# Optimization experiments

Measured on AMD Instinct MI355X. Metric: run time of the kernel, lower is better.

## Reference

```python
import jax, jax.numpy as jnp
import numpy as np

D_MODEL = 512
D_FFN = 2048
N_LAYERS = 6
VOCAB = 1000
D_STATE = 16
D_CONV = 4
D_INNER = 2 * D_MODEL  # expand=2
DT_RANK = 32           # ceil(d_model/16)
B, LT, LS = 2, 512, 512


def _pos_encoding(length, d_model):
    pos = np.arange(length, dtype=np.float32)[:, None]
    div = np.exp(np.arange(0, d_model, 2, dtype=np.float32) * (-np.log(10000.0) / d_model))
    pe = np.zeros((length, d_model), np.float32)
    pe[:, 0::2] = np.sin(pos * div)
    pe[:, 1::2] = np.cos(pos * div)
    return jnp.asarray(pe)


def _layer_norm(x, g, b, eps=1e-6):
    m = x.mean(-1, keepdims=True)
    v = ((x - m) ** 2).mean(-1, keepdims=True)
    return (x - m) * jax.lax.rsqrt(v + eps) * g + b


def _mamba(x, in_w, conv_w, conv_b, xproj_w, dt_w, dt_b, A_log, Dskip, out_w):
    # x: (b, l, d_model)
    b, l, _ = x.shape
    xz = x @ in_w.T                                   # (b, l, 2*d_inner)
    xc, z = jnp.split(xz, 2, axis=-1)
    # causal depthwise conv over time
    xt = jnp.transpose(xc, (0, 2, 1))                 # (b, d_inner, l)
    xt = jnp.pad(xt, ((0, 0), (0, 0), (D_CONV - 1, 0)))
    xt = jax.lax.conv_general_dilated(
        xt, conv_w, window_strides=(1,), padding='VALID',
        feature_group_count=D_INNER, dimension_numbers=('NCH', 'OIH', 'NCH'))
    xc = jax.nn.silu(jnp.transpose(xt, (0, 2, 1)) + conv_b)  # (b, l, d_inner)
    dbl = xc @ xproj_w.T                              # (b, l, dt_rank + 2*n)
    dt, Bm, Cm = jnp.split(dbl, [DT_RANK, DT_RANK + D_STATE], axis=-1)
    dt = jax.nn.softplus(dt @ dt_w.T + dt_b)          # (b, l, d_inner)
    A = -jnp.exp(A_log)                               # (d_inner, n)

    def step(h, xs):
        dt_t, B_t, C_t, u_t = xs                      # (b,d),(b,n),(b,n),(b,d)
        dA = jnp.exp(dt_t[..., None] * A)             # (b, d, n)
        h = dA * h + (dt_t * u_t)[..., None] * B_t[:, None, :]
        y = jnp.einsum('bdn,bn->bd', h, C_t)
        return h, y

    h0 = jnp.zeros((b, D_INNER, D_STATE), x.dtype)
    xs = (jnp.swapaxes(dt, 0, 1), jnp.swapaxes(Bm, 0, 1),
          jnp.swapaxes(Cm, 0, 1), jnp.swapaxes(xc, 0, 1))
    _, ys = jax.lax.scan(step, h0, xs)                # ys: (l, b, d_inner)
    y = jnp.swapaxes(ys, 0, 1) + xc * Dskip
    y = y * jax.nn.silu(z)
    return y @ out_w.T                                # (b, l, d_model)


def setup_inputs() -> dict:
    key = jax.random.key(0)
    ks = iter(jax.random.split(key, 40))

    def rn(shape, s=0.02):
        return jax.random.normal(next(ks), shape, jnp.float32) * s

    def mamba_params():
        return dict(
            in_w=rn((N_LAYERS, 2 * D_INNER, D_MODEL)),
            conv_w=rn((N_LAYERS, D_INNER, 1, D_CONV), 0.1),
            conv_b=rn((N_LAYERS, D_INNER)),
            xproj=rn((N_LAYERS, DT_RANK + 2 * D_STATE, D_INNER)),
            dtw=rn((N_LAYERS, D_INNER, DT_RANK)),
            dtb=rn((N_LAYERS, D_INNER)),
            Alog=jnp.log(jnp.broadcast_to(jnp.arange(1.0, D_STATE + 1.0, dtype=jnp.float32), (N_LAYERS, D_INNER, D_STATE))),
            D=jnp.ones((N_LAYERS, D_INNER), jnp.float32),
            outw=rn((N_LAYERS, D_MODEL, D_INNER)),
        )

    ps, pc = mamba_params(), mamba_params()
    inp = {
        'src': jax.random.normal(next(ks), (B, LS, D_MODEL), jnp.float32),
        'tgt': jax.random.randint(next(ks), (B, LT), 0, VOCAB),
        'emb': rn((VOCAB, D_MODEL)),
        'in_w_s': ps['in_w'], 'conv_w_s': ps['conv_w'], 'conv_b_s': ps['conv_b'],
        'xproj_s': ps['xproj'], 'dtw_s': ps['dtw'], 'dtb_s': ps['dtb'],
        'Alog_s': ps['Alog'], 'D_s': ps['D'], 'outw_s': ps['outw'],
        'in_w_c': pc['in_w'], 'conv_w_c': pc['conv_w'], 'conv_b_c': pc['conv_b'],
        'xproj_c': pc['xproj'], 'dtw_c': pc['dtw'], 'dtb_c': pc['dtb'],
        'Alog_c': pc['Alog'], 'D_c': pc['D'], 'outw_c': pc['outw'],
        'ffn_w1': rn((N_LAYERS, D_FFN, D_MODEL)),
        'ffn_b1': jnp.zeros((N_LAYERS, D_FFN), jnp.float32),
        'ffn_w2': rn((N_LAYERS, D_MODEL, D_FFN)),
        'ffn_b2': jnp.zeros((N_LAYERS, D_MODEL), jnp.float32),
        'ln_g': jnp.ones((N_LAYERS, 3, D_MODEL), jnp.float32),
        'ln_b': jnp.zeros((N_LAYERS, 3, D_MODEL), jnp.float32),
        'fin_g': jnp.ones((D_MODEL,), jnp.float32),
        'fin_b': jnp.zeros((D_MODEL,), jnp.float32),
    }
    return inp


def reference(src, tgt, emb, in_w_s, conv_w_s, conv_b_s, xproj_s, dtw_s, dtb_s,
              Alog_s, D_s, outw_s, in_w_c, conv_w_c, conv_b_c, xproj_c, dtw_c,
              dtb_c, Alog_c, D_c, outw_c, ffn_w1, ffn_b1, ffn_w2, ffn_b2,
              ln_g, ln_b, fin_g, fin_b):
    # NormalizedEmbedding + sinusoidal positional encoding
    x = emb[tgt] * jnp.sqrt(jnp.asarray(D_MODEL, jnp.float32))
    x = x + _pos_encoding(LT, D_MODEL)[None]
    for i in range(N_LAYERS):
        # self mamba (post-norm, normalize_before=False)
        t2 = _mamba(x, in_w_s[i], conv_w_s[i], conv_b_s[i], xproj_s[i],
                    dtw_s[i], dtb_s[i], Alog_s[i], D_s[i], outw_s[i])
        x = _layer_norm(x + t2, ln_g[i, 0], ln_b[i, 0])
        # cross mamba over concat([memory, tgt]) then take last LT steps
        cat = jnp.concatenate([src, x], axis=1)
        t2 = _mamba(cat, in_w_c[i], conv_w_c[i], conv_b_c[i], xproj_c[i],
                    dtw_c[i], dtb_c[i], Alog_c[i], D_c[i], outw_c[i])[:, -LT:]
        x = _layer_norm(x + t2, ln_g[i, 1], ln_b[i, 1])
        # positionwise FFN
        h = jax.nn.relu(x @ ffn_w1[i].T + ffn_b1[i]) @ ffn_w2[i].T + ffn_b2[i]
        x = _layer_norm(x + h, ln_g[i, 2], ln_b[i, 2])
    return _layer_norm(x, fin_g, fin_b)
```

## Files before the change

### kernel.cpp

```cpp
#include <hip/hip_runtime.h>
#include <math.h>

#define DMODEL 512
#define DINNER 1024
#define DSTATE 16
#define DTRANK 32
#define NLAYERS 6
#define BB 2
#define LT 512
#define LS 512
#define NCHUNK 32

typedef __attribute__((ext_vector_type(8))) short bf16x8;
typedef __attribute__((ext_vector_type(8))) unsigned short u16x8;
typedef __attribute__((ext_vector_type(4))) float f32x4;

__device__ __forceinline__ unsigned short f2bf(float f) {
  unsigned u = __float_as_uint(f);
  u += 0x7fffu + ((u >> 16) & 1u);
  return (unsigned short)(u >> 16);
}

template<int EPI>
__device__ __forceinline__ float epi_apply(float acc, float b) {
  if (EPI == 1) { float v = acc + b; return v > 0.f ? v : 0.f; }
  if (EPI == 2) { return acc + b; }
  if (EPI == 3) { float v = acc + b; return fmaxf(v, 0.f) + log1pf(__expf(-fabsf(v))); }
  return acc;
}

__global__ __launch_bounds__(256) void cvt_kernel(const float* __restrict__ in,
    unsigned short* __restrict__ out, int n8) {
  int i = blockIdx.x * 256 + threadIdx.x;
  if (i >= n8) return;
  float4 a = ((const float4*)in)[i * 2];
  float4 b = ((const float4*)in)[i * 2 + 1];
  u16x8 o;
  o[0] = f2bf(a.x); o[1] = f2bf(a.y); o[2] = f2bf(a.z); o[3] = f2bf(a.w);
  o[4] = f2bf(b.x); o[5] = f2bf(b.y); o[6] = f2bf(b.z); o[7] = f2bf(b.w);
  *(u16x8*)&out[i * 8] = o;
}

__global__ __launch_bounds__(256) void embed_kernel(const int* __restrict__ tgt,
    const float* __restrict__ emb, float* __restrict__ X,
    unsigned short* __restrict__ Xb) {
  int i = blockIdx.x * 256 + threadIdx.x;
  int d = i & (DMODEL - 1);
  int bt = i >> 9;
  int t = bt & (LT - 1);
  int tok = tgt[bt];
  float div = __expf((float)(d & ~1) * (-9.210340371976184f / (float)DMODEL));
  float ang = (float)t * div;
  float pe = (d & 1) ? cosf(ang) : sinf(ang);
  float v = emb[(size_t)tok * DMODEL + d] * 22.627416997969522f + pe;
  X[i] = v;
  Xb[i] = f2bf(v);
}

__global__ __launch_bounds__(256) void concat_kernel(const float* __restrict__ src,
    const float* __restrict__ X, unsigned short* __restrict__ CATb) {
  int i = blockIdx.x * 256 + threadIdx.x;
  int c8 = (i & 63) * 8;
  int r = i >> 6;
  int l = r & 1023;
  int b = r >> 10;
  const float* s = (l < LS) ? (src + ((size_t)b * LS + l) * DMODEL)
                            : (X + ((size_t)b * LT + (l - LS)) * DMODEL);
  float4 a = *(const float4*)(s + c8);
  float4 bq = *(const float4*)(s + c8 + 4);
  u16x8 o;
  o[0] = f2bf(a.x); o[1] = f2bf(a.y); o[2] = f2bf(a.z); o[3] = f2bf(a.w);
  o[4] = f2bf(bq.x); o[5] = f2bf(bq.y); o[6] = f2bf(bq.z); o[7] = f2bf(bq.w);
  *(u16x8*)&CATb[(size_t)r * DMODEL + c8] = o;
}

template<int BK, int EPI, bool SPLIT, bool OUTB>
__global__ __launch_bounds__(256) void mgemm(
    const unsigned short* __restrict__ A, const unsigned short* __restrict__ Bw,
    const float* __restrict__ bias, float* __restrict__ C,
    unsigned short* __restrict__ Cb, int M, int N, int K, int lda) {
  constexpr int PAD = BK + 8;
  constexpr int CH = BK / 32;
  __shared__ __align__(16) unsigned short As[64 * PAD];
  __shared__ __align__(16) unsigned short Bs[64 * PAD];
  const int tid = threadIdx.x;
  const int bn = blockIdx.x * 64;
  const int bm = blockIdx.y * 64;
  const int lane = tid & 63;
  const int w = tid >> 6;
  const int wr = (w >> 1) * 32;
  const int wc = (w & 1) * 32;
  const int l15 = lane & 15;
  const int l4 = lane >> 4;
  const int koff = l4 * 8;
  int kcnt = K, kbeg = 0;
  if (SPLIT) { kcnt = K / (int)gridDim.z; kbeg = blockIdx.z * kcnt; }
  const int nt = kcnt / BK;
  f32x4 acc[2][2] = {};

  int row_[CH], k8_[CH];
  const unsigned short *Ap[CH], *Bp[CH];
#pragma unroll
  for (int i = 0; i < CH; ++i) {
    int f = tid + 256 * i;
    row_[i] = f / (BK / 8);
    k8_[i] = (f % (BK / 8)) * 8;
    Ap[i] = A + (size_t)(bm + row_[i]) * lda + kbeg + k8_[i];
    Bp[i] = Bw + (size_t)(bn + row_[i]) * K + kbeg + k8_[i];
  }

  u16x8 av[CH], bv[CH];
#pragma unroll
  for (int i = 0; i < CH; ++i) { av[i] = *(const u16x8*)Ap[i]; bv[i] = *(const u16x8*)Bp[i]; }

  for (int t = 0; t < nt; ++t) {
    __syncthreads();
#pragma unroll
    for (int i = 0; i < CH; ++i) {
      *(u16x8*)&As[row_[i] * PAD + k8_[i]] = av[i];
      *(u16x8*)&Bs[row_[i] * PAD + k8_[i]] = bv[i];
    }
    if (t + 1 < nt) {
      int ko = (t + 1) * BK;
#pragma unroll
      for (int i = 0; i < CH; ++i) {
        av[i] = *(const u16x8*)(Ap[i] + ko);
        bv[i] = *(const u16x8*)(Bp[i] + ko);
      }
    }
    __syncthreads();
#pragma unroll
    for (int kk = 0; kk < CH; ++kk) {
      bf16x8 afr[2], bfr[2];
#pragma unroll
      for (int i = 0; i < 2; ++i) {
        afr[i] = *(const bf16x8*)&As[(wr + i * 16 + l15) * PAD + kk * 32 + koff];
        bfr[i] = *(const bf16x8*)&Bs[(wc + i * 16 + l15) * PAD + kk * 32 + koff];
      }
#pragma unroll
      for (int fr = 0; fr < 2; ++fr)
#pragma unroll
        for (int fc = 0; fc < 2; ++fc)
          acc[fr][fc] = __builtin_amdgcn_mfma_f32_16x16x32_bf16(
              afr[fr], bfr[fc], acc[fr][fc], 0, 0, 0);
    }
  }

  if (SPLIT) {
    float* Pz = C + (size_t)blockIdx.z * M * N;
#pragma unroll
    for (int fc = 0; fc < 2; ++fc) {
      int col = bn + wc + fc * 16 + l15;
#pragma unroll
      for (int fr = 0; fr < 2; ++fr) {
        int row0 = bm + wr + fr * 16 + l4 * 4;
#pragma unroll
        for (int r = 0; r < 4; ++r)
          Pz[(size_t)(row0 + r) * N + col] = acc[fr][fc][r];
      }
    }
  } else {
#pragma unroll
    for (int fc = 0; fc < 2; ++fc) {
      int col = bn + wc + fc * 16 + l15;
      float bvs = (EPI != 0) ? bias[col] : 0.f;
#pragma unroll
      for (int fr = 0; fr < 2; ++fr) {
        int row0 = bm + wr + fr * 16 + l4 * 4;
#pragma unroll
        for (int r = 0; r < 4; ++r) {
          float v = epi_apply<EPI>(acc[fr][fc][r], bvs);
          if (OUTB) Cb[(size_t)(row0 + r) * N + col] = f2bf(v);
          else      C[(size_t)(row0 + r) * N + col] = v;
        }
      }
    }
  }
}

__global__ __launch_bounds__(256) void xred_kernel(const float* __restrict__ P,
    float* __restrict__ DBL, unsigned short* __restrict__ DBLb, int total) {
  int i = blockIdx.x * 256 + threadIdx.x;
  if (i >= total) return;
  float s = 0.f;
  for (int z = 0; z < 8; ++z) s += P[(size_t)z * total + i];
  DBL[i] = s;
  int col = i & 63;
  if (col < 32) DBLb[(size_t)(i >> 6) * 32 + col] = f2bf(s);
}

__global__ __launch_bounds__(256) void conv_silu_kernel(
    const float* __restrict__ xz, const float* __restrict__ w,
    const float* __restrict__ bias, float* __restrict__ out,
    unsigned short* __restrict__ outb, int L) {
  int idx = blockIdx.x * 256 + threadIdx.x;
  int d = idx & (DINNER - 1);
  int bt = idx >> 10;
  int b = bt / L;
  int t = bt - b * L;
  const float* col = xz + ((size_t)b * L) * (2 * DINNER) + d;
  float acc = bias[d];
#pragma unroll
  for (int k = 0; k < 4; ++k) {
    int tt = t - 3 + k;
    if (tt >= 0) acc = fmaf(col[(size_t)tt * (2 * DINNER)], w[d * 4 + k], acc);
  }
  float sig = 1.f / (1.f + __expf(-acc));
  float v = acc * sig;
  out[idx] = v;
  outb[idx] = f2bf(v);
}

__global__ __launch_bounds__(256) void scan_pass1(
    const float* __restrict__ dt, const float* __restrict__ dbl,
    const float* __restrict__ u, const float* __restrict__ Alog,
    float* __restrict__ P, float* __restrict__ S, int L, int CL) {
  __shared__ float BC[32][32];
  const int tid = threadIdx.x;
  const int d = blockIdx.x * 256 + tid;
  const int b = blockIdx.y;
  const int c = blockIdx.z;
  const int t0 = c * CL;
  if (tid < CL * 8) {
    int t = tid >> 3, j4 = (tid & 7) * 4;
    *(float4*)&BC[t][j4] = *(const float4*)(dbl + ((size_t)b * L + t0 + t) * 64 + 32 + j4);
  }
  float A[16], h[16], Pp[16];
#pragma unroll
  for (int j = 0; j < 4; ++j) {
    float4 a4 = *(const float4*)(Alog + d * 16 + j * 4);
    A[j * 4 + 0] = -__expf(a4.x); A[j * 4 + 1] = -__expf(a4.y);
    A[j * 4 + 2] = -__expf(a4.z); A[j * 4 + 3] = -__expf(a4.w);
  }
#pragma unroll
  for (int n = 0; n < 16; ++n) { h[n] = 0.f; Pp[n] = 1.f; }
  const float* dtp = dt + ((size_t)b * L + t0) * DINNER + d;
  const float* up  = u  + ((size_t)b * L + t0) * DINNER + d;
  __syncthreads();
  float dtv = dtp[0], uv = up[0];
  for (int t = 0; t < CL; ++t) {
    float dtn = 0.f, un = 0.f;
    if (t + 1 < CL) { dtn = dtp[(size_t)(t + 1) * DINNER]; un = up[(size_t)(t + 1) * DINNER]; }
    float du = dtv * uv;
    float Bv[16];
#pragma unroll
    for (int j = 0; j < 4; ++j) {
      float4 b4 = *(const float4*)&BC[t][j * 4];
      Bv[j * 4 + 0] = b4.x; Bv[j * 4 + 1] = b4.y; Bv[j * 4 + 2] = b4.z; Bv[j * 4 + 3] = b4.w;
    }
#pragma unroll
    for (int n = 0; n < 16; ++n) {
      float dA = __expf(dtv * A[n]);
      Pp[n] *= dA;
      h[n] = fmaf(dA, h[n], du * Bv[n]);
    }
    dtv = dtn; uv = un;
  }
  size_t base = (size_t)c * 32768 + ((size_t)(b * 1024 + d) << 4);
#pragma unroll
  for (int j = 0; j < 4; ++j) {
    *(float4*)&P[base + j * 4] = make_float4(Pp[j*4], Pp[j*4+1], Pp[j*4+2], Pp[j*4+3]);
    *(float4*)&S[base + j * 4] = make_float4(h[j*4], h[j*4+1], h[j*4+2], h[j*4+3]);
  }
}

__global__ __launch_bounds__(256) void scan_mid(
    const float* __restrict__ P, const float* __restrict__ S,
    float* __restrict__ HIN, int C) {
  int s = blockIdx.x * 256 + threadIdx.x;
  float h = 0.f;
  for (int c = 0; c < C; ++c) {
    float p = P[(size_t)c * 32768 + s];
    float sv = S[(size_t)c * 32768 + s];
    HIN[(size_t)c * 32768 + s] = h;
    h = fmaf(p, h, sv);
  }
}

__global__ __launch_bounds__(256) void scan_pass2(
    const float* __restrict__ dt, const float* __restrict__ dbl,
    const float* __restrict__ u, const float* __restrict__ xz,
    const float* __restrict__ Alog, const float* __restrict__ Dsk,
    const float* __restrict__ HIN, unsigned short* __restrict__ ysb,
    int L, int CL, int c0) {
  __shared__ float BC[32][32];
  const int tid = threadIdx.x;
  const int d = blockIdx.x * 256 + tid;
  const int b = blockIdx.y;
  const int c = blockIdx.z + c0;
  const int t0 = c * CL;
  if (tid < CL * 8) {
    int t = tid >> 3, j4 = (tid & 7) * 4;
    *(float4*)&BC[t][j4] = *(const float4*)(dbl + ((size_t)b * L + t0 + t) * 64 + 32 + j4);
  }
  float A[16], h[16];
#pragma unroll
  for (int j = 0; j < 4; ++j) {
    float4 a4 = *(const float4*)(Alog + d * 16 + j * 4);
    A[j * 4 + 0] = -__expf(a4.x); A[j * 4 + 1] = -__expf(a4.y);
    A[j * 4 + 2] = -__expf(a4.z); A[j * 4 + 3] = -__expf(a4.w);
  }
  size_t base = (size_t)c * 32768 + ((size_t)(b * 1024 + d) << 4);
#pragma unroll
  for (int j = 0; j < 4; ++j) {
    float4 h4 = *(const float4*)&HIN[base + j * 4];
    h[j * 4 + 0] = h4.x; h[j * 4 + 1] = h4.y; h[j * 4 + 2] = h4.z; h[j * 4 + 3] = h4.w;
  }
  float Dv = Dsk[d];
  const float* dtp = dt + ((size_t)b * L + t0) * DINNER + d;
  const float* up  = u  + ((size_t)b * L + t0) * DINNER + d;
  const float* zp  = xz + ((size_t)b * L + t0) * (2 * DINNER) + DINNER + d;
  unsigned short* yp = ysb + ((size_t)(b * 512) + (t0 - c0 * CL)) * DINNER + d;
  __syncthreads();
  float dtv = dtp[0], uv = up[0], zv = zp[0];
  for (int t = 0; t < CL; ++t) {
    float dtn = 0.f, un = 0.f, zn = 0.f;
    if (t + 1 < CL) {
      dtn = dtp[(size_t)(t + 1) * DINNER];
      un  = up[(size_t)(t + 1) * DINNER];
      zn  = zp[(size_t)(t + 1) * (2 * DINNER)];
    }
    float du = dtv * uv;
    float Bv[16], Cv[16];
#pragma unroll
    for (int j = 0; j < 4; ++j) {
      float4 b4 = *(const float4*)&BC[t][j * 4];
      float4 c4 = *(const float4*)&BC[t][16 + j * 4];
      Bv[j*4+0] = b4.x; Bv[j*4+1] = b4.y; Bv[j*4+2] = b4.z; Bv[j*4+3] = b4.w;
      Cv[j*4+0] = c4.x; Cv[j*4+1] = c4.y; Cv[j*4+2] = c4.z; Cv[j*4+3] = c4.w;
    }
    float y = 0.f;
#pragma unroll
    for (int n = 0; n < 16; ++n) {
      float dA = __expf(dtv * A[n]);
      h[n] = fmaf(dA, h[n], du * Bv[n]);
      y = fmaf(h[n], Cv[n], y);
    }
    float sig = 1.f / (1.f + __expf(-zv));
    yp[(size_t)t * DINNER] = f2bf((y + uv * Dv) * (zv * sig));
    dtv = dtn; uv = un; zv = zn;
  }
}

template<int NZ, int EPI>
__global__ __launch_bounds__(64) void ln_red_kernel(
    const float* __restrict__ res, const float* __restrict__ P,
    const float* __restrict__ bias, const float* __restrict__ g,
    const float* __restrict__ be, float* __restrict__ out,
    unsigned short* __restrict__ outb) {
  int r = blockIdx.x;
  int lane = threadIdx.x;
  const float* rp = res + (size_t)r * DMODEL;
  float v[8];
  float s = 0.f, ss = 0.f;
#pragma unroll
  for (int j = 0; j < 8; ++j) {
    int col = lane + j * 64;
    float acc = 0.f;
#pragma unroll
    for (int z = 0; z < NZ; ++z) acc += P[(size_t)z * 524288 + (size_t)r * DMODEL + col];
    float bv = (EPI != 0) ? bias[col] : 0.f;
    float x = rp[col] + epi_apply<EPI>(acc, bv);
    v[j] = x; s += x; ss += x * x;
  }
#pragma unroll
  for (int o = 32; o > 0; o >>= 1) { s += __shfl_xor(s, o); ss += __shfl_xor(ss, o); }
  float m = s * (1.f / 512.f);
  float var = ss * (1.f / 512.f) - m * m;
  float rs = rsqrtf(var + 1e-6f);
#pragma unroll
  for (int j = 0; j < 8; ++j) {
    int col = lane + j * 64;
    float o2 = (v[j] - m) * rs * g[col] + be[col];
    out[(size_t)r * DMODEL + col] = o2;
    outb[(size_t)r * DMODEL + col] = f2bf(o2);
  }
}

__global__ __launch_bounds__(64) void ln_final_kernel(
    const float* __restrict__ res, const float* __restrict__ g,
    const float* __restrict__ be, float* __restrict__ out) {
  int r = blockIdx.x;
  int lane = threadIdx.x;
  const float* rp = res + (size_t)r * DMODEL;
  float v[8];
  float s = 0.f, ss = 0.f;
#pragma unroll
  for (int j = 0; j < 8; ++j) {
    float x = rp[lane + j * 64];
    v[j] = x; s += x; ss += x * x;
  }
#pragma unroll
  for (int o = 32; o > 0; o >>= 1) { s += __shfl_xor(s, o); ss += __shfl_xor(ss, o); }
  float m = s * (1.f / 512.f);
  float var = ss * (1.f / 512.f) - m * m;
  float rs = rsqrtf(var + 1e-6f);
#pragma unroll
  for (int j = 0; j < 8; ++j) {
    int c = lane + j * 64;
    out[(size_t)r * DMODEL + c] = (v[j] - m) * rs * g[c] + be[c];
  }
}

extern "C" void kernel_launch(void* const* d_in, const int* in_sizes, int n_in,
                              void* d_out, int out_size, void* d_ws, size_t ws_size,
                              hipStream_t stream) {
  (void)in_sizes; (void)n_in; (void)out_size; (void)ws_size;
  const float* src      = (const float*)d_in[0];
  const int*   tgt      = (const int*)d_in[1];
  const float* emb      = (const float*)d_in[2];
  const float* in_w_s   = (const float*)d_in[3];
  const float* conv_w_s = (const float*)d_in[4];
  const float* conv_b_s = (const float*)d_in[5];
  const float* xproj_s  = (const float*)d_in[6];
  const float* dtw_s    = (const float*)d_in[7];
  const float* dtb_s    = (const float*)d_in[8];
  const float* Alog_s   = (const float*)d_in[9];
  const float* D_s      = (const float*)d_in[10];
  const float* outw_s   = (const float*)d_in[11];
  const float* in_w_c   = (const float*)d_in[12];
  const float* conv_w_c = (const float*)d_in[13];
  const float* conv_b_c = (const float*)d_in[14];
  const float* xproj_c  = (const float*)d_in[15];
  const float* dtw_c    = (const float*)d_in[16];
  const float* dtb_c    = (const float*)d_in[17];
  const float* Alog_c   = (const float*)d_in[18];
  const float* D_c      = (const float*)d_in[19];
  const float* outw_c   = (const float*)d_in[20];
  const float* ffn_w1   = (const float*)d_in[21];
  const float* ffn_b1   = (const float*)d_in[22];
  const float* ffn_w2   = (const float*)d_in[23];
  const float* ffn_b2   = (const float*)d_in[24];
  const float* ln_g     = (const float*)d_in[25];
  const float* ln_b     = (const float*)d_in[26];
  const float* fin_g    = (const float*)d_in[27];
  const float* fin_b    = (const float*)d_in[28];

  float* ws   = (float*)d_ws;
  float* X    = ws;
  float* XZ   = X + 524288;
  float* XC   = XZ + 4194304;
  float* DT   = XC + 2097152;
  float* DBL  = DT + 2097152;
  float* SC_P = DBL + 131072;
  float* SC_S = SC_P + 1048576;
  unsigned short* U = (unsigned short*)(SC_S + 1048576);
  unsigned short* Xb   = U;
  unsigned short* CATb = Xb + 524288;
  unsigned short* XCb  = CATb + 1048576;
  unsigned short* DBLb = XCb + 2097152;
  unsigned short* XZb  = DBLb + 65536;
  unsigned short* YSb  = XZb + 2097152;
  unsigned short* WB   = YSb + 1048576;
  unsigned short* inwsb = WB;
  unsigned short* inwcb = inwsb + 6291456;
  unsigned short* xpsb  = inwcb + 6291456;
  unsigned short* xpcb  = xpsb + 393216;
  unsigned short* dtwsb = xpcb + 393216;
  unsigned short* dtwcb = dtwsb + 196608;
  unsigned short* owsb  = dtwcb + 196608;
  unsigned short* owcb  = owsb + 3145728;
  unsigned short* f1b   = owcb + 3145728;
  unsigned short* f2b   = f1b + 6291456;

  cvt_kernel<<<3072, 256, 0, stream>>>(in_w_s, inwsb, 786432);
  cvt_kernel<<<3072, 256, 0, stream>>>(in_w_c, inwcb, 786432);
  cvt_kernel<<<192, 256, 0, stream>>>(xproj_s, xpsb, 49152);
  cvt_kernel<<<192, 256, 0, stream>>>(xproj_c, xpcb, 49152);
  cvt_kernel<<<96, 256, 0, stream>>>(dtw_s, dtwsb, 24576);
  cvt_kernel<<<96, 256, 0, stream>>>(dtw_c, dtwcb, 24576);
  cvt_kernel<<<1536, 256, 0, stream>>>(outw_s, owsb, 393216);
  cvt_kernel<<<1536, 256, 0, stream>>>(outw_c, owcb, 393216);
  cvt_kernel<<<3072, 256, 0, stream>>>(ffn_w1, f1b, 786432);
  cvt_kernel<<<3072, 256, 0, stream>>>(ffn_w2, f2b, 786432);

  embed_kernel<<<2048, 256, 0, stream>>>(tgt, emb, X, Xb);

  for (int i = 0; i < NLAYERS; ++i) {
    mgemm<64, 0, false, false><<<dim3(32, 16), 256, 0, stream>>>(
        Xb, inwsb + (size_t)i * 1048576, nullptr, XZ, nullptr, 1024, 2048, 512, 512);
    conv_silu_kernel<<<4096, 256, 0, stream>>>(
        XZ, conv_w_s + (size_t)i * 4096, conv_b_s + (size_t)i * 1024, XC, XCb, 512);
    mgemm<64, 0, true, false><<<dim3(1, 16, 8), 256, 0, stream>>>(
        XCb, xpsb + (size_t)i * 65536, nullptr, SC_P, nullptr, 1024, 64, 1024, 1024);
    xred_kernel<<<256, 256, 0, stream>>>(SC_P, DBL, DBLb, 65536);
    mgemm<32, 3, false, false><<<dim3(16, 16), 256, 0, stream>>>(
        DBLb, dtwsb + (size_t)i * 32768, dtb_s + (size_t)i * 1024, DT, nullptr,
        1024, 1024, 32, 32);
    scan_pass1<<<dim3(4, 2, 32), 256, 0, stream>>>(
        DT, DBL, XC, Alog_s + (size_t)i * 16384, SC_P, SC_S, 512, 16);
    scan_mid<<<128, 256, 0, stream>>>(SC_P, SC_S, SC_P, 32);
    scan_pass2<<<dim3(4, 2, 32), 256, 0, stream>>>(
        DT, DBL, XC, XZ, Alog_s + (size_t)i * 16384, D_s + (size_t)i * 1024,
        SC_P, YSb, 512, 16, 0);
    mgemm<64, 0, true, false><<<dim3(8, 16, 4), 256, 0, stream>>>(
        YSb, owsb + (size_t)i * 524288, nullptr, XZ, nullptr, 1024, 512, 1024, 1024);
    ln_red_kernel<4, 0><<<1024, 64, 0, stream>>>(
        X, XZ, nullptr, ln_g + (size_t)(i * 3 + 0) * 512,
        ln_b + (size_t)(i * 3 + 0) * 512, X, Xb);

    concat_kernel<<<512, 256, 0, stream>>>(src, X, CATb);
    mgemm<64, 0, false, false><<<dim3(32, 32), 256, 0, stream>>>(
        CATb, inwcb + (size_t)i * 1048576, nullptr, XZ, nullptr, 2048, 2048, 512, 512);
    conv_silu_kernel<<<8192, 256, 0, stream>>>(
        XZ, conv_w_c + (size_t)i * 4096, conv_b_c + (size_t)i * 1024, XC, XCb, 1024);
    mgemm<64, 0, true, false><<<dim3(1, 32, 8), 256, 0, stream>>>(
        XCb, xpcb + (size_t)i * 65536, nullptr, SC_P, nullptr, 2048, 64, 1024, 1024);
    xred_kernel<<<512, 256, 0, stream>>>(SC_P, DBL, DBLb, 131072);
    mgemm<32, 3, false, false><<<dim3(16, 32), 256, 0, stream>>>(
        DBLb, dtwcb + (size_t)i * 32768, dtb_c + (size_t)i * 1024, DT, nullptr,
        2048, 1024, 32, 32);
    scan_pass1<<<dim3(4, 2, 32), 256, 0, stream>>>(
        DT, DBL, XC, Alog_c + (size_t)i * 16384, SC_P, SC_S, 1024, 32);
    scan_mid<<<128, 256, 0, stream>>>(SC_P, SC_S, SC_P, 32);
    scan_pass2<<<dim3(4, 2, 16), 256, 0, stream>>>(
        DT, DBL, XC, XZ, Alog_c + (size_t)i * 16384, D_c + (size_t)i * 1024,
        SC_P, YSb, 1024, 32, 16);
    mgemm<64, 0, true, false><<<dim3(8, 16, 4), 256, 0, stream>>>(
        YSb, owcb + (size_t)i * 524288, nullptr, XZ, nullptr, 1024, 512, 1024, 1024);
    ln_red_kernel<4, 0><<<1024, 64, 0, stream>>>(
        X, XZ, nullptr, ln_g + (size_t)(i * 3 + 1) * 512,
        ln_b + (size_t)(i * 3 + 1) * 512, X, Xb);

    mgemm<64, 1, false, true><<<dim3(32, 16), 256, 0, stream>>>(
        Xb, f1b + (size_t)i * 1048576, ffn_b1 + (size_t)i * 2048, nullptr, XZb,
        1024, 2048, 512, 512);
    mgemm<64, 0, true, false><<<dim3(8, 16, 8), 256, 0, stream>>>(
        XZb, f2b + (size_t)i * 1048576, nullptr, XZ, nullptr, 1024, 512, 2048, 2048);
    ln_red_kernel<8, 2><<<1024, 64, 0, stream>>>(
        X, XZ, ffn_b2 + (size_t)i * 512, ln_g + (size_t)(i * 3 + 2) * 512,
        ln_b + (size_t)(i * 3 + 2) * 512, X, Xb);
  }

  ln_final_kernel<<<1024, 64, 0, stream>>>(X, fin_g, fin_b, (float*)d_out);
}
```

Before: 1.223 ms.

## Store intermediates in bf16, widen GEMM tiles, fuse weight conversion and scan mid-pass

Intermediate activations (xz, conv output, dt, dbl) are now stored as bf16 rather than fp32, which halves memory traffic in the conv, scan and GEMM epilogues. A new 64x128-tile GEMM variant replaces the 64x64 one for the large projections. The ten weight-conversion launches are merged into a single kernel. The separate scan_mid launch is removed, and each scan_pass2 block instead recomputes its own carry-in state from the per-chunk P/S values. The concat kernel is removed: src is copied once and the layernorm writes x straight into the concat buffer. Together these cut launches and bandwidth, at the cost of redundant carry recomputation and lower-precision intermediates.

```diff
diff --git a/kernel.cpp b/kernel.cpp
--- a/kernel.cpp
+++ b/kernel.cpp
@@ -9,7 +9,6 @@
 #define BB 2
 #define LT 512
 #define LS 512
-#define NCHUNK 32
 
 typedef __attribute__((ext_vector_type(8))) short bf16x8;
 typedef __attribute__((ext_vector_type(8))) unsigned short u16x8;
@@ -19,6 +18,9 @@
   unsigned u = __float_as_uint(f);
   u += 0x7fffu + ((u >> 16) & 1u);
   return (unsigned short)(u >> 16);
+}
+__device__ __forceinline__ float bf2f(unsigned short u) {
+  return __uint_as_float((unsigned)u << 16);
 }
 
 template<int EPI>
@@ -29,16 +31,32 @@
   return acc;
 }
 
-__global__ __launch_bounds__(256) void cvt_kernel(const float* __restrict__ in,
-    unsigned short* __restrict__ out, int n8) {
+__global__ __launch_bounds__(256) void cvt_all_kernel(
+    const float* __restrict__ i0, const float* __restrict__ i1,
+    const float* __restrict__ i2, const float* __restrict__ i3,
+    const float* __restrict__ i4, const float* __restrict__ i5,
+    const float* __restrict__ i6, const float* __restrict__ i7,
+    const float* __restrict__ i8, const float* __restrict__ i9,
+    unsigned short* __restrict__ outbase) {
   int i = blockIdx.x * 256 + threadIdx.x;
-  if (i >= n8) return;
-  float4 a = ((const float4*)in)[i * 2];
-  float4 b = ((const float4*)in)[i * 2 + 1];
+  if (i >= 4079616) return;
+  const float* in; int off;
+  if      (i <  786432) { in = i0; off = i; }
+  else if (i < 1572864) { in = i1; off = i -  786432; }
+  else if (i < 1622016) { in = i2; off = i - 1572864; }
+  else if (i < 1671168) { in = i3; off = i - 1622016; }
+  else if (i < 1695744) { in = i4; off = i - 1671168; }
+  else if (i < 1720320) { in = i5; off = i - 1695744; }
+  else if (i < 2113536) { in = i6; off = i - 1720320; }
+  else if (i < 2506752) { in = i7; off = i - 2113536; }
+  else if (i < 3293184) { in = i8; off = i - 2506752; }
+  else                  { in = i9; off = i - 3293184; }
+  float4 a = ((const float4*)in)[off * 2];
+  float4 b = ((const float4*)in)[off * 2 + 1];
   u16x8 o;
   o[0] = f2bf(a.x); o[1] = f2bf(a.y); o[2] = f2bf(a.z); o[3] = f2bf(a.w);
   o[4] = f2bf(b.x); o[5] = f2bf(b.y); o[6] = f2bf(b.z); o[7] = f2bf(b.w);
-  *(u16x8*)&out[i * 8] = o;
+  *(u16x8*)&outbase[(size_t)i * 8] = o;
 }
 
 __global__ __launch_bounds__(256) void embed_kernel(const int* __restrict__ tgt,
@@ -57,21 +75,133 @@
   Xb[i] = f2bf(v);
 }
 
-__global__ __launch_bounds__(256) void concat_kernel(const float* __restrict__ src,
-    const float* __restrict__ X, unsigned short* __restrict__ CATb) {
+__global__ __launch_bounds__(256) void catsrc_kernel(const float* __restrict__ src,
+    unsigned short* __restrict__ CATb) {
   int i = blockIdx.x * 256 + threadIdx.x;
   int c8 = (i & 63) * 8;
   int r = i >> 6;
-  int l = r & 1023;
-  int b = r >> 10;
-  const float* s = (l < LS) ? (src + ((size_t)b * LS + l) * DMODEL)
-                            : (X + ((size_t)b * LT + (l - LS)) * DMODEL);
-  float4 a = *(const float4*)(s + c8);
-  float4 bq = *(const float4*)(s + c8 + 4);
+  int b = r >> 9, l = r & 511;
+  const float* s = src + ((size_t)b * 512 + l) * DMODEL + c8;
+  float4 a = *(const float4*)s;
+  float4 bq = *(const float4*)(s + 4);
   u16x8 o;
   o[0] = f2bf(a.x); o[1] = f2bf(a.y); o[2] = f2bf(a.z); o[3] = f2bf(a.w);
   o[4] = f2bf(bq.x); o[5] = f2bf(bq.y); o[6] = f2bf(bq.z); o[7] = f2bf(bq.w);
-  *(u16x8*)&CATb[(size_t)r * DMODEL + c8] = o;
+  *(u16x8*)&CATb[((size_t)b * 1024 + l) * DMODEL + c8] = o;
+}
+
+template<int BK, int EPI, bool SPLIT, bool OUTB>
+__global__ __launch_bounds__(256) void mgemmA(
+    const unsigned short* __restrict__ A, const unsigned short* __restrict__ Bw,
+    const float* __restrict__ bias, float* __restrict__ C,
+    unsigned short* __restrict__ Cb, int M, int N, int K, int lda) {
+  constexpr int PAD = BK + 8;
+  constexpr int CHA = BK / 32;
+  constexpr int CHB = BK / 16;
+  __shared__ __align__(16) unsigned short As[64 * PAD];
+  __shared__ __align__(16) unsigned short Bs[128 * PAD];
+  const int tid = threadIdx.x;
+  const int bn = blockIdx.x * 128;
+  const int bm = blockIdx.y * 64;
+  const int lane = tid & 63;
+  const int w = tid >> 6;
+  const int wr = (w >> 1) * 32;
+  const int wc = (w & 1) * 64;
+  const int l15 = lane & 15;
+  const int l4 = lane >> 4;
+  const int koff = l4 * 8;
+  int kcnt = K, kbeg = 0;
+  if (SPLIT) { kcnt = K / (int)gridDim.z; kbeg = blockIdx.z * kcnt; }
+  const int nt = kcnt / BK;
+  f32x4 acc[2][4] = {};
+
+  int arow_[CHA], ak8_[CHA];
+  const unsigned short* Ap[CHA];
+#pragma unroll
+  for (int i = 0; i < CHA; ++i) {
+    int f = tid + 256 * i;
+    arow_[i] = f / (BK / 8);
+    ak8_[i] = (f % (BK / 8)) * 8;
+    Ap[i] = A + (size_t)(bm + arow_[i]) * lda + kbeg + ak8_[i];
+  }
+  int brow_[CHB], bk8_[CHB];
+  const unsigned short* Bp[CHB];
+#pragma unroll
+  for (int i = 0; i < CHB; ++i) {
+    int f = tid + 256 * i;
+    brow_[i] = f / (BK / 8);
+    bk8_[i] = (f % (BK / 8)) * 8;
+    Bp[i] = Bw + (size_t)(bn + brow_[i]) * K + kbeg + bk8_[i];
+  }
+
+  u16x8 av[CHA], bv[CHB];
+#pragma unroll
+  for (int i = 0; i < CHA; ++i) av[i] = *(const u16x8*)Ap[i];
+#pragma unroll
+  for (int i = 0; i < CHB; ++i) bv[i] = *(const u16x8*)Bp[i];
+
+  for (int t = 0; t < nt; ++t) {
+    __syncthreads();
+#pragma unroll
+    for (int i = 0; i < CHA; ++i) *(u16x8*)&As[arow_[i] * PAD + ak8_[i]] = av[i];
+#pragma unroll
+    for (int i = 0; i < CHB; ++i) *(u16x8*)&Bs[brow_[i] * PAD + bk8_[i]] = bv[i];
+    if (t + 1 < nt) {
+      int ko = (t + 1) * BK;
+#pragma unroll
+      for (int i = 0; i < CHA; ++i) av[i] = *(const u16x8*)(Ap[i] + ko);
+#pragma unroll
+      for (int i = 0; i < CHB; ++i) bv[i] = *(const u16x8*)(Bp[i] + ko);
+    }
+    __syncthreads();
+#pragma unroll
+    for (int kk = 0; kk < BK / 32; ++kk) {
+      bf16x8 afr[2], bfr[4];
+#pragma unroll
+      for (int i = 0; i < 2; ++i)
+        afr[i] = *(const bf16x8*)&As[(wr + i * 16 + l15) * PAD + kk * 32 + koff];
+#pragma unroll
+      for (int j = 0; j < 4; ++j)
+        bfr[j] = *(const bf16x8*)&Bs[(wc + j * 16 + l15) * PAD + kk * 32 + koff];
+#pragma unroll
+      for (int fr = 0; fr < 2; ++fr)
+#pragma unroll
+        for (int fc = 0; fc < 4; ++fc)
+          acc[fr][fc] = __builtin_amdgcn_mfma_f32_16x16x32_bf16(
+              afr[fr], bfr[fc], acc[fr][fc], 0, 0, 0);
+    }
+  }
+
+  if (SPLIT) {
+    float* Pz = C + (size_t)blockIdx.z * M * N;
+#pragma unroll
+    for (int fc = 0; fc < 4; ++fc) {
+      int col = bn + wc + fc * 16 + l15;
+#pragma unroll
+      for (int fr = 0; fr < 2; ++fr) {
+        int row0 = bm + wr + fr * 16 + l4 * 4;
+#pragma unroll
+        for (int r = 0; r < 4; ++r)
+          Pz[(size_t)(row0 + r) * N + col] = acc[fr][fc][r];
+      }
+    }
+  } else {
+#pragma unroll
+    for (int fc = 0; fc < 4; ++fc) {
+      int col = bn + wc + fc * 16 + l15;
+      float bvs = (EPI != 0) ? bias[col] : 0.f;
+#pragma unroll
+      for (int fr = 0; fr < 2; ++fr) {
+        int row0 = bm + wr + fr * 16 + l4 * 4;
+#pragma unroll
+        for (int r = 0; r < 4; ++r) {
+          float v = epi_apply<EPI>(acc[fr][fc][r], bvs);
+          if (OUTB) Cb[(size_t)(row0 + r) * N + col] = f2bf(v);
+          else      C[(size_t)(row0 + r) * N + col] = v;
+        }
+      }
+    }
+  }
 }
 
 template<int BK, int EPI, bool SPLIT, bool OUTB>
@@ -179,41 +309,36 @@
 }
 
 __global__ __launch_bounds__(256) void xred_kernel(const float* __restrict__ P,
-    float* __restrict__ DBL, unsigned short* __restrict__ DBLb, int total) {
+    unsigned short* __restrict__ DBLb, int total) {
   int i = blockIdx.x * 256 + threadIdx.x;
   if (i >= total) return;
   float s = 0.f;
   for (int z = 0; z < 8; ++z) s += P[(size_t)z * total + i];
-  DBL[i] = s;
-  int col = i & 63;
-  if (col < 32) DBLb[(size_t)(i >> 6) * 32 + col] = f2bf(s);
+  DBLb[i] = f2bf(s);
 }
 
 __global__ __launch_bounds__(256) void conv_silu_kernel(
-    const float* __restrict__ xz, const float* __restrict__ w,
-    const float* __restrict__ bias, float* __restrict__ out,
-    unsigned short* __restrict__ outb, int L) {
+    const unsigned short* __restrict__ xzb, const float* __restrict__ w,
+    const float* __restrict__ bias, unsigned short* __restrict__ outb, int L) {
   int idx = blockIdx.x * 256 + threadIdx.x;
   int d = idx & (DINNER - 1);
   int bt = idx >> 10;
   int b = bt / L;
   int t = bt - b * L;
-  const float* col = xz + ((size_t)b * L) * (2 * DINNER) + d;
+  const unsigned short* col = xzb + ((size_t)b * L) * (2 * DINNER) + d;
   float acc = bias[d];
 #pragma unroll
   for (int k = 0; k < 4; ++k) {
     int tt = t - 3 + k;
-    if (tt >= 0) acc = fmaf(col[(size_t)tt * (2 * DINNER)], w[d * 4 + k], acc);
+    if (tt >= 0) acc = fmaf(bf2f(col[(size_t)tt * (2 * DINNER)]), w[d * 4 + k], acc);
   }
   float sig = 1.f / (1.f + __expf(-acc));
-  float v = acc * sig;
-  out[idx] = v;
-  outb[idx] = f2bf(v);
+  outb[idx] = f2bf(acc * sig);
 }
 
 __global__ __launch_bounds__(256) void scan_pass1(
-    const float* __restrict__ dt, const float* __restrict__ dbl,
-    const float* __restrict__ u, const float* __restrict__ Alog,
+    const unsigned short* __restrict__ dt, const unsigned short* __restrict__ dblb,
+    const unsigned short* __restrict__ u, const float* __restrict__ Alog,
     float* __restrict__ P, float* __restrict__ S, int L, int CL) {
   __shared__ float BC[32][32];
   const int tid = threadIdx.x;
@@ -221,9 +346,11 @@
   const int b = blockIdx.y;
   const int c = blockIdx.z;
   const int t0 = c * CL;
-  if (tid < CL * 8) {
-    int t = tid >> 3, j4 = (tid & 7) * 4;
-    *(float4*)&BC[t][j4] = *(const float4*)(dbl + ((size_t)b * L + t0 + t) * 64 + 32 + j4);
+  if (tid < CL * 4) {
+    int t = tid >> 2, j8 = (tid & 3) * 8;
+    u16x8 v = *(const u16x8*)(dblb + ((size_t)b * L + t0 + t) * 64 + 32 + j8);
+#pragma unroll
+    for (int j = 0; j < 8; ++j) BC[t][j8 + j] = bf2f(v[j]);
   }
   float A[16], h[16], Pp[16];
 #pragma unroll
@@ -234,25 +361,22 @@
   }
 #pragma unroll
   for (int n = 0; n < 16; ++n) { h[n] = 0.f; Pp[n] = 1.f; }
-  const float* dtp = dt + ((size_t)b * L + t0) * DINNER + d;
-  const float* up  = u  + ((size_t)b * L + t0) * DINNER + d;
+  const unsigned short* dtp = dt + ((size_t)b * L + t0) * DINNER + d;
+  const unsigned short* up  = u  + ((size_t)b * L + t0) * DINNER + d;
   __syncthreads();
-  float dtv = dtp[0], uv = up[0];
+  float dtv = bf2f(dtp[0]), uv = bf2f(up[0]);
   for (int t = 0; t < CL; ++t) {
     float dtn = 0.f, un = 0.f;
-    if (t + 1 < CL) { dtn = dtp[(size_t)(t + 1) * DINNER]; un = up[(size_t)(t + 1) * DINNER]; }
+    if (t + 1 < CL) {
+      dtn = bf2f(dtp[(size_t)(t + 1) * DINNER]);
+      un  = bf2f(up[(size_t)(t + 1) * DINNER]);
+    }
     float du = dtv * uv;
-    float Bv[16];
-#pragma unroll
-    for (int j = 0; j < 4; ++j) {
-      float4 b4 = *(const float4*)&BC[t][j * 4];
-      Bv[j * 4 + 0] = b4.x; Bv[j * 4 + 1] = b4.y; Bv[j * 4 + 2] = b4.z; Bv[j * 4 + 3] = b4.w;
-    }
 #pragma unroll
     for (int n = 0; n < 16; ++n) {
       float dA = __expf(dtv * A[n]);
       Pp[n] *= dA;
-      h[n] = fmaf(dA, h[n], du * Bv[n]);
+      h[n] = fmaf(dA, h[n], du * BC[t][n]);
     }
     dtv = dtn; uv = un;
   }
@@ -264,34 +388,23 @@
   }
 }
 
-__global__ __launch_bounds__(256) void scan_mid(
+__global__ __launch_bounds__(256) void scan_pass2(
+    const unsigned short* __restrict__ dt, const unsigned short* __restrict__ dblb,
+    const unsigned short* __restrict__ u, const unsigned short* __restrict__ xzb,
+    const float* __restrict__ Alog, const float* __restrict__ Dsk,
     const float* __restrict__ P, const float* __restrict__ S,
-    float* __restrict__ HIN, int C) {
-  int s = blockIdx.x * 256 + threadIdx.x;
-  float h = 0.f;
-  for (int c = 0; c < C; ++c) {
-    float p = P[(size_t)c * 32768 + s];
-    float sv = S[(size_t)c * 32768 + s];
-    HIN[(size_t)c * 32768 + s] = h;
-    h = fmaf(p, h, sv);
-  }
-}
-
-__global__ __launch_bounds__(256) void scan_pass2(
-    const float* __restrict__ dt, const float* __restrict__ dbl,
-    const float* __restrict__ u, const float* __restrict__ xz,
-    const float* __restrict__ Alog, const float* __restrict__ Dsk,
-    const float* __restrict__ HIN, unsigned short* __restrict__ ysb,
-    int L, int CL, int c0) {
+    unsigned short* __restrict__ ysb, int L, int CL, int c0) {
   __shared__ float BC[32][32];
   const int tid = threadIdx.x;
   const int d = blockIdx.x * 256 + tid;
   const int b = blockIdx.y;
   const int c = blockIdx.z + c0;
   const int t0 = c * CL;
-  if (tid < CL * 8) {
-    int t = tid >> 3, j4 = (tid & 7) * 4;
-    *(float4*)&BC[t][j4] = *(const float4*)(dbl + ((size_t)b * L + t0 + t) * 64 + 32 + j4);
+  if (tid < CL * 4) {
+    int t = tid >> 2, j8 = (tid & 3) * 8;
+    u16x8 v = *(const u16x8*)(dblb + ((size_t)b * L + t0 + t) * 64 + 32 + j8);
+#pragma unroll
+    for (int j = 0; j < 8; ++j) BC[t][j8 + j] = bf2f(v[j]);
   }
   float A[16], h[16];
 #pragma unroll
@@ -300,41 +413,42 @@
     A[j * 4 + 0] = -__expf(a4.x); A[j * 4 + 1] = -__expf(a4.y);
     A[j * 4 + 2] = -__expf(a4.z); A[j * 4 + 3] = -__expf(a4.w);
   }
-  size_t base = (size_t)c * 32768 + ((size_t)(b * 1024 + d) << 4);
-#pragma unroll
-  for (int j = 0; j < 4; ++j) {
-    float4 h4 = *(const float4*)&HIN[base + j * 4];
-    h[j * 4 + 0] = h4.x; h[j * 4 + 1] = h4.y; h[j * 4 + 2] = h4.z; h[j * 4 + 3] = h4.w;
+#pragma unroll
+  for (int n = 0; n < 16; ++n) h[n] = 0.f;
+  size_t sbase = (size_t)(b * 1024 + d) << 4;
+  for (int cc = 0; cc < c; ++cc) {
+    size_t bb = (size_t)cc * 32768 + sbase;
+#pragma unroll
+    for (int j = 0; j < 4; ++j) {
+      float4 p4 = *(const float4*)&P[bb + j * 4];
+      float4 s4 = *(const float4*)&S[bb + j * 4];
+      h[j*4+0] = fmaf(p4.x, h[j*4+0], s4.x);
+      h[j*4+1] = fmaf(p4.y, h[j*4+1], s4.y);
+      h[j*4+2] = fmaf(p4.z, h[j*4+2], s4.z);
+      h[j*4+3] = fmaf(p4.w, h[j*4+3], s4.w);
+    }
   }
   float Dv = Dsk[d];
-  const float* dtp = dt + ((size_t)b * L + t0) * DINNER + d;
-  const float* up  = u  + ((size_t)b * L + t0) * DINNER + d;
-  const float* zp  = xz + ((size_t)b * L + t0) * (2 * DINNER) + DINNER + d;
+  const unsigned short* dtp = dt + ((size_t)b * L + t0) * DINNER + d;
+  const unsigned short* up  = u  + ((size_t)b * L + t0) * DINNER + d;
+  const unsigned short* zp  = xzb + ((size_t)b * L + t0) * (2 * DINNER) + DINNER + d;
   unsigned short* yp = ysb + ((size_t)(b * 512) + (t0 - c0 * CL)) * DINNER + d;
   __syncthreads();
-  float dtv = dtp[0], uv = up[0], zv = zp[0];
+  float dtv = bf2f(dtp[0]), uv = bf2f(up[0]), zv = bf2f(zp[0]);
   for (int t = 0; t < CL; ++t) {
     float dtn = 0.f, un = 0.f, zn = 0.f;
     if (t + 1 < CL) {
-      dtn = dtp[(size_t)(t + 1) * DINNER];
-      un  = up[(size_t)(t + 1) * DINNER];
-      zn  = zp[(size_t)(t + 1) * (2 * DINNER)];
+      dtn = bf2f(dtp[(size_t)(t + 1) * DINNER]);
+      un  = bf2f(up[(size_t)(t + 1) * DINNER]);
+      zn  = bf2f(zp[(size_t)(t + 1) * (2 * DINNER)]);
     }
     float du = dtv * uv;
-    float Bv[16], Cv[16];
-#pragma unroll
-    for (int j = 0; j < 4; ++j) {
-      float4 b4 = *(const float4*)&BC[t][j * 4];
-      float4 c4 = *(const float4*)&BC[t][16 + j * 4];
-      Bv[j*4+0] = b4.x; Bv[j*4+1] = b4.y; Bv[j*4+2] = b4.z; Bv[j*4+3] = b4.w;
-      Cv[j*4+0] = c4.x; Cv[j*4+1] = c4.y; Cv[j*4+2] = c4.z; Cv[j*4+3] = c4.w;
-    }
     float y = 0.f;
 #pragma unroll
     for (int n = 0; n < 16; ++n) {
       float dA = __expf(dtv * A[n]);
-      h[n] = fmaf(dA, h[n], du * Bv[n]);
-      y = fmaf(h[n], Cv[n], y);
+      h[n] = fmaf(dA, h[n], du * BC[t][n]);
+      y = fmaf(h[n], BC[t][16 + n], y);
     }
     float sig = 1.f / (1.f + __expf(-zv));
     yp[(size_t)t * DINNER] = f2bf((y + uv * Dv) * (zv * sig));
@@ -347,10 +461,12 @@
     const float* __restrict__ res, const float* __restrict__ P,
     const float* __restrict__ bias, const float* __restrict__ g,
     const float* __restrict__ be, float* __restrict__ out,
-    unsigned short* __restrict__ outb) {
+    unsigned short* __restrict__ outb, int row_scale, int row_off) {
   int r = blockIdx.x;
+  int b = r >> 9, t = r & 511;
   int lane = threadIdx.x;
   const float* rp = res + (size_t)r * DMODEL;
+  size_t ob = ((size_t)(b * row_scale + row_off + t)) * DMODEL;
   float v[8];
   float s = 0.f, ss = 0.f;
 #pragma unroll
@@ -373,7 +489,7 @@
     int col = lane + j * 64;
     float o2 = (v[j] - m) * rs * g[col] + be[col];
     out[(size_t)r * DMODEL + col] = o2;
-    outb[(size_t)r * DMODEL + col] = f2bf(o2);
+    outb[ob + col] = f2bf(o2);
   }
 }
 
@@ -439,19 +555,17 @@
   float* ws   = (float*)d_ws;
   float* X    = ws;
   float* XZ   = X + 524288;
-  float* XC   = XZ + 4194304;
-  float* DT   = XC + 2097152;
-  float* DBL  = DT + 2097152;
-  float* SC_P = DBL + 131072;
+  float* SC_P = XZ + 4194304;
   float* SC_S = SC_P + 1048576;
   unsigned short* U = (unsigned short*)(SC_S + 1048576);
   unsigned short* Xb   = U;
   unsigned short* CATb = Xb + 524288;
   unsigned short* XCb  = CATb + 1048576;
   unsigned short* DBLb = XCb + 2097152;
-  unsigned short* XZb  = DBLb + 65536;
-  unsigned short* YSb  = XZb + 2097152;
-  unsigned short* WB   = YSb + 1048576;
+  unsigned short* XZb  = DBLb + 131072;
+  unsigned short* YSb  = XZb + 4194304;
+  unsigned short* DTb  = YSb + 1048576;
+  unsigned short* WB   = DTb + 2097152;
   unsigned short* inwsb = WB;
   unsigned short* inwcb = inwsb + 6291456;
   unsigned short* xpsb  = inwcb + 6291456;
@@ -463,73 +577,63 @@
   unsigned short* f1b   = owcb + 3145728;
   unsigned short* f2b   = f1b + 6291456;
 
-  cvt_kernel<<<3072, 256, 0, stream>>>(in_w_s, inwsb, 786432);
-  cvt_kernel<<<3072, 256, 0, stream>>>(in_w_c, inwcb, 786432);
-  cvt_kernel<<<192, 256, 0, stream>>>(xproj_s, xpsb, 49152);
-  cvt_kernel<<<192, 256, 0, stream>>>(xproj_c, xpcb, 49152);
-  cvt_kernel<<<96, 256, 0, stream>>>(dtw_s, dtwsb, 24576);
-  cvt_kernel<<<96, 256, 0, stream>>>(dtw_c, dtwcb, 24576);
-  cvt_kernel<<<1536, 256, 0, stream>>>(outw_s, owsb, 393216);
-  cvt_kernel<<<1536, 256, 0, stream>>>(outw_c, owcb, 393216);
-  cvt_kernel<<<3072, 256, 0, stream>>>(ffn_w1, f1b, 786432);
-  cvt_kernel<<<3072, 256, 0, stream>>>(ffn_w2, f2b, 786432);
-
+  cvt_all_kernel<<<15936, 256, 0, stream>>>(
+      in_w_s, in_w_c, xproj_s, xproj_c, dtw_s, dtw_c, outw_s, outw_c,
+      ffn_w1, ffn_w2, WB);
   embed_kernel<<<2048, 256, 0, stream>>>(tgt, emb, X, Xb);
+  catsrc_kernel<<<256, 256, 0, stream>>>(src, CATb);
 
   for (int i = 0; i < NLAYERS; ++i) {
-    mgemm<64, 0, false, false><<<dim3(32, 16), 256, 0, stream>>>(
-        Xb, inwsb + (size_t)i * 1048576, nullptr, XZ, nullptr, 1024, 2048, 512, 512);
+    mgemmA<64, 0, false, true><<<dim3(16, 16), 256, 0, stream>>>(
+        Xb, inwsb + (size_t)i * 1048576, nullptr, nullptr, XZb, 1024, 2048, 512, 512);
     conv_silu_kernel<<<4096, 256, 0, stream>>>(
-        XZ, conv_w_s + (size_t)i * 4096, conv_b_s + (size_t)i * 1024, XC, XCb, 512);
+        XZb, conv_w_s + (size_t)i * 4096, conv_b_s + (size_t)i * 1024, XCb, 512);
     mgemm<64, 0, true, false><<<dim3(1, 16, 8), 256, 0, stream>>>(
         XCb, xpsb + (size_t)i * 65536, nullptr, SC_P, nullptr, 1024, 64, 1024, 1024);
-    xred_kernel<<<256, 256, 0, stream>>>(SC_P, DBL, DBLb, 65536);
-    mgemm<32, 3, false, false><<<dim3(16, 16), 256, 0, stream>>>(
-        DBLb, dtwsb + (size_t)i * 32768, dtb_s + (size_t)i * 1024, DT, nullptr,
-        1024, 1024, 32, 32);
+    xred_kernel<<<256, 256, 0, stream>>>(SC_P, DBLb, 65536);
+    mgemm<32, 3, false, true><<<dim3(16, 16), 256, 0, stream>>>(
+        DBLb, dtwsb + (size_t)i * 32768, dtb_s + (size_t)i * 1024, nullptr, DTb,
+        1024, 1024, 32, 64);
     scan_pass1<<<dim3(4, 2, 32), 256, 0, stream>>>(
-        DT, DBL, XC, Alog_s + (size_t)i * 16384, SC_P, SC_S, 512, 16);
-    scan_mid<<<128, 256, 0, stream>>>(SC_P, SC_S, SC_P, 32);
+        DTb, DBLb, XCb, Alog_s + (size_t)i * 16384, SC_P, SC_S, 512, 16);
     scan_pass2<<<dim3(4, 2, 32), 256, 0, stream>>>(
-        DT, DBL, XC, XZ, Alog_s + (size_t)i * 16384, D_s + (size_t)i * 1024,
-        SC_P, YSb, 512, 16, 0);
-    mgemm<64, 0, true, false><<<dim3(8, 16, 4), 256, 0, stream>>>(
+        DTb, DBLb, XCb, XZb, Alog_s + (size_t)i * 16384, D_s + (size_t)i * 1024,
+        SC_P, SC_S, YSb, 512, 16, 0);
+    mgemmA<64, 0, true, false><<<dim3(4, 16, 4), 256, 0, stream>>>(
         YSb, owsb + (size_t)i * 524288, nullptr, XZ, nullptr, 1024, 512, 1024, 1024);
     ln_red_kernel<4, 0><<<1024, 64, 0, stream>>>(
         X, XZ, nullptr, ln_g + (size_t)(i * 3 + 0) * 512,
-        ln_b + (size_t)(i * 3 + 0) * 512, X, Xb);
-
-    concat_kernel<<<512, 256, 0, stream>>>(src, X, CATb);
-    mgemm<64, 0, false, false><<<dim3(32, 32), 256, 0, stream>>>(
-        CATb, inwcb + (size_t)i * 1048576, nullptr, XZ, nullptr, 2048, 2048, 512, 512);
+        ln_b + (size_t)(i * 3 + 0) * 512, X, CATb, 1024, 512);
+
+    mgemmA<64, 0, false, true><<<dim3(16, 32), 256, 0, stream>>>(
+        CATb, inwcb + (size_t)i * 1048576, nullptr, nullptr, XZb, 2048, 2048, 512, 512);
     conv_silu_kernel<<<8192, 256, 0, stream>>>(
-        XZ, conv_w_c + (size_t)i * 4096, conv_b_c + (size_t)i * 1024, XC, XCb, 1024);
+        XZb, conv_w_c + (size_t)i * 4096, conv_b_c + (size_t)i * 1024, XCb, 1024);
     mgemm<64, 0, true, false><<<dim3(1, 32, 8), 256, 0, stream>>>(
         XCb, xpcb + (size_t)i * 65536, nullptr, SC_P, nullptr, 2048, 64, 1024, 1024);
-    xred_kernel<<<512, 256, 0, stream>>>(SC_P, DBL, DBLb, 131072);
-    mgemm<32, 3, false, false><<<dim3(16, 32), 256, 0, stream>>>(
-        DBLb, dtwcb + (size_t)i * 32768, dtb_c + (size_t)i * 1024, DT, nullptr,
-        2048, 1024, 32, 32);
+    xred_kernel<<<512, 256, 0, stream>>>(SC_P, DBLb, 131072);
+    mgemm<32, 3, false, true><<<dim3(16, 32), 256, 0, stream>>>(
+        DBLb, dtwcb + (size_t)i * 32768, dtb_c + (size_t)i * 1024, nullptr, DTb,
+        2048, 1024, 32, 64);
     scan_pass1<<<dim3(4, 2, 32), 256, 0, stream>>>(
-        DT, DBL, XC, Alog_c + (size_t)i * 16384, SC_P, SC_S, 1024, 32);
-    scan_mid<<<128, 256, 0, stream>>>(SC_P, SC_S, SC_P, 32);
+        DTb, DBLb, XCb, Alog_c + (size_t)i * 16384, SC_P, SC_S, 1024, 32);
     scan_pass2<<<dim3(4, 2, 16), 256, 0, stream>>>(
-        DT, DBL, XC, XZ, Alog_c + (size_t)i * 16384, D_c + (size_t)i * 1024,
-        SC_P, YSb, 1024, 32, 16);
-    mgemm<64, 0, true, false><<<dim3(8, 16, 4), 256, 0, stream>>>(
+        DTb, DBLb, XCb, XZb, Alog_c + (size_t)i * 16384, D_c + (size_t)i * 1024,
+        SC_P, SC_S, YSb, 1024, 32, 16);
+    mgemmA<64, 0, true, false><<<dim3(4, 16, 4), 256, 0, stream>>>(
         YSb, owcb + (size_t)i * 524288, nullptr, XZ, nullptr, 1024, 512, 1024, 1024);
     ln_red_kernel<4, 0><<<1024, 64, 0, stream>>>(
         X, XZ, nullptr, ln_g + (size_t)(i * 3 + 1) * 512,
-        ln_b + (size_t)(i * 3 + 1) * 512, X, Xb);
-
-    mgemm<64, 1, false, true><<<dim3(32, 16), 256, 0, stream>>>(
+        ln_b + (size_t)(i * 3 + 1) * 512, X, Xb, 512, 0);
+
+    mgemmA<64, 1, false, true><<<dim3(16, 16), 256, 0, stream>>>(
         Xb, f1b + (size_t)i * 1048576, ffn_b1 + (size_t)i * 2048, nullptr, XZb,
         1024, 2048, 512, 512);
-    mgemm<64, 0, true, false><<<dim3(8, 16, 8), 256, 0, stream>>>(
+    mgemmA<64, 0, true, false><<<dim3(4, 16, 8), 256, 0, stream>>>(
         XZb, f2b + (size_t)i * 1048576, nullptr, XZ, nullptr, 1024, 512, 2048, 2048);
     ln_red_kernel<8, 2><<<1024, 64, 0, stream>>>(
         X, XZ, ffn_b2 + (size_t)i * 512, ln_g + (size_t)(i * 3 + 2) * 512,
-        ln_b + (size_t)(i * 3 + 2) * 512, X, Xb);
+        ln_b + (size_t)(i * 3 + 2) * 512, X, Xb, 512, 0);
   }
 
   ln_final_kernel<<<1024, 64, 0, stream>>>(X, fin_g, fin_b, (float*)d_out);
```

Result: faster. 1.194 ms (-2.4%).
